# Kernel optimization log

Measured on AMD Instinct MI355X. Metric: run time of the kernel, lower is better.

## Reference

```python
import jax, jax.numpy as jnp
import numpy as np
import math

LMAX = 2
NUM_Z = 4
N_NODES = 20000
N_GRAPHS = 5000
N_EDGES = 320000
# irreps as (mul, l, parity)
IR_SH   = [(1, 0, 1), (1, 1, -1), (1, 2, 1)]
IR_ATTR = [(NUM_Z**2, 0, 1), (NUM_Z**2, 1, -1), (NUM_Z**2, 2, 1)]
IR_MID  = [(64, 0, 1), (24, 1, 1), (24, 1, -1), (16, 2, 1), (16, 2, -1)]
IR_OUT  = [(1, 0, -1), (6, 0, 1)]


def _cg(j1, j2, j3, m1, m2, m3):
    if m1 + m2 != m3:
        return 0.0
    f = math.factorial
    pre = math.sqrt((2 * j3 + 1) * f(j3 + j1 - j2) * f(j3 - j1 + j2) * f(j1 + j2 - j3) / f(j1 + j2 + j3 + 1))
    pre *= math.sqrt(f(j3 + m3) * f(j3 - m3) * f(j1 - m1) * f(j1 + m1) * f(j2 - m2) * f(j2 + m2))
    s = 0.0
    for k in range(max(0, j2 - j3 - m1, j1 - j3 + m2), min(j1 + j2 - j3, j1 - m1, j2 + m2) + 1):
        s += (-1) ** k / (f(k) * f(j1 + j2 - j3 - k) * f(j1 - m1 - k) * f(j2 + m2 - k) * f(j3 - j2 + m1 + k) * f(j3 - j1 - m2 + k))
    return pre * s


def _u(l):
    # complex -> real spherical harmonics change of basis, m = -l..l
    U = np.zeros((2 * l + 1, 2 * l + 1), dtype=complex)
    for m in range(-l, l + 1):
        if m > 0:
            U[m + l, -m + l] = 1 / math.sqrt(2)
            U[m + l, m + l] = (-1) ** m / math.sqrt(2)
        elif m == 0:
            U[l, l] = 1.0
        else:
            U[m + l, m + l] = 1j / math.sqrt(2)
            U[m + l, -m + l] = -1j * (-1) ** (-m) / math.sqrt(2)
    return U


def _w3j(l1, l2, l3):
    C = np.zeros((2 * l1 + 1, 2 * l2 + 1, 2 * l3 + 1))
    for m1 in range(-l1, l1 + 1):
        for m2 in range(-l2, l2 + 1):
            m3 = m1 + m2
            if -l3 <= m3 <= l3:
                C[m1 + l1, m2 + l2, m3 + l3] = _cg(l1, l2, l3, m1, m2, m3)
    T = np.einsum('am,bn,co,mno->abc', _u(l1), _u(l2), _u(l3).conj(), C.astype(complex))
    T = T.real if np.abs(T.real).max() >= np.abs(T.imag).max() else T.imag
    return (T / np.linalg.norm(T)).astype(np.float32)  # Frobenius norm 1, e3nn convention


W3J = {(a, b, c): _w3j(a, b, c) for a in range(3) for b in range(3) for c in range(3) if abs(a - b) <= c <= a + b}


def _slices(ir):
    s = [0]
    for m, l, _ in ir:
        s.append(s[-1] + m * (2 * l + 1))
    return s


def _paths(ir1, ir2, iro):
    paths = []
    fan = [0] * len(iro)
    off = 0
    for a, (m1, l1, p1) in enumerate(ir1):
        for b, (m2, l2, p2) in enumerate(ir2):
            for c, (m3, l3, p3) in enumerate(iro):
                if p1 * p2 == p3 and abs(l1 - l2) <= l3 <= l1 + l2:
                    paths.append((a, b, c, off))
                    fan[c] += m1 * m2
                    off += m1 * m2 * m3
    return paths, fan, off


def _fctp(x1, x2, w, ir1, ir2, iro):
    # FullyConnectedTensorProduct: 'uvw' weighted Clebsch-Gordan contraction per path
    s1, s2 = _slices(ir1), _slices(ir2)
    paths, fan, _ = _paths(ir1, ir2, iro)
    E = x1.shape[0]
    out = [jnp.zeros((E, m * (2 * l + 1)), x1.dtype) for m, l, _ in iro]
    for a, b, c, off in paths:
        m1, l1, _ = ir1[a]
        m2, l2, _ = ir2[b]
        m3, l3, _ = iro[c]
        W = w[off:off + m1 * m2 * m3].reshape(m1, m2, m3)
        C = jnp.asarray(W3J[(l1, l2, l3)], x1.dtype)
        xa = x1[:, s1[a]:s1[a + 1]].reshape(E, m1, 2 * l1 + 1)
        xb = x2[:, s2[b]:s2[b + 1]].reshape(E, m2, 2 * l2 + 1)
        alpha = math.sqrt(2 * l3 + 1) / math.sqrt(fan[c])
        y = jnp.einsum('eui,evj,ijk,uvw->ewk', xa, xb, C, W)
        out[c] = out[c] + (alpha * y).reshape(E, -1)
    return jnp.concatenate(out, axis=1)


def _sh(v):
    # component-normalized harmonic polynomials for l=0,1,2 (normalize=False)
    x, y, z = v[:, 0], v[:, 1], v[:, 2]
    r2 = x * x + y * y + z * z
    s3, s15, s5 = math.sqrt(3.0), math.sqrt(15.0), math.sqrt(5.0)
    sh1 = s3 * jnp.stack([y, z, x], axis=1)
    sh2 = jnp.stack([s15 * x * y, s15 * y * z, 0.5 * s5 * (3 * z * z - r2), s15 * x * z, 0.5 * s15 * (x * x - y * y)], axis=1)
    return jnp.concatenate([jnp.ones_like(x)[:, None], sh1, sh2], axis=1)  # [E, 9]


def _forward(pos, w_tp1, w_tp2, z, batch, edge_src, edge_dst):
    E = edge_src.shape[0]
    ev = pos[edge_src] - pos[edge_dst]
    sh = _sh(ev)
    zz = NUM_Z * z[edge_src] + z[edge_dst]
    zzf = jax.nn.one_hot(zz, NUM_Z ** 2, dtype=sh.dtype) * NUM_Z  # [E, 16]
    # 'uvu' TensorProduct of (16x0e) with sh: outer product per l block
    blocks = [(0, 1), (1, 4), (4, 9)]
    edge_attr = jnp.concatenate([(zzf[:, :, None] * sh[:, None, a:b]).reshape(E, -1) for a, b in blocks], axis=1)
    inv_nn = 1.0 / math.sqrt(3.0)  # num_neighbors = 3
    node = jax.ops.segment_sum(sh, edge_dst, num_segments=N_NODES) * inv_nn
    ef = _fctp(node[edge_src], edge_attr, w_tp1, IR_SH, IR_ATTR, IR_MID)
    node = jax.ops.segment_sum(ef, edge_dst, num_segments=N_NODES) * inv_nn
    ef = _fctp(node[edge_src], edge_attr, w_tp2, IR_MID, IR_ATTR, IR_OUT)
    node = jax.ops.segment_sum(ef, edge_dst, num_segments=N_NODES) * inv_nn
    return jax.ops.segment_sum(node, batch, num_segments=N_GRAPHS) * 0.5  # num_nodes = 4


def setup_inputs() -> dict:
    key = jax.random.key(0)
    k = jax.random.split(key, 7)
    _, _, n1 = _paths(IR_SH, IR_ATTR, IR_MID)
    _, _, n2 = _paths(IR_MID, IR_ATTR, IR_OUT)
    return {
        'pos': jax.random.normal(k[0], (N_NODES, 3), jnp.float32),
        'z': jax.random.randint(k[1], (N_NODES,), 0, NUM_Z, jnp.int32),
        'batch': jnp.sort(jax.random.randint(k[2], (N_NODES,), 0, N_GRAPHS, jnp.int32)),
        'edge_src': jax.random.randint(k[3], (N_EDGES,), 0, N_NODES, jnp.int32),
        'edge_dst': jax.random.randint(k[4], (N_EDGES,), 0, N_NODES, jnp.int32),
        'w_tp1': jax.random.normal(k[5], (n1,), jnp.float32),
        'w_tp2': jax.random.normal(k[6], (n2,), jnp.float32),
    }


def reference(pos, z, batch, edge_src, edge_dst, w_tp1, w_tp2):
    return _forward(pos, w_tp1, w_tp2, z, batch, edge_src, edge_dst)
```

## Files before the change

### kernel.cpp

```cpp
#include <hip/hip_runtime.h>


#define N_EDGES   320000
#define NN_NODES  20000
#define NN_GRAPHS 5000

__device__ __forceinline__ void sh_from_vec(float x, float y, float z,
                                            float* B1, float* B2) {
    const float s3   = 1.7320508075688772f;
    const float s15  = 3.8729833462074170f;
    const float s5h  = 1.1180339887498949f;
    const float s15h = 1.9364916731037085f;
    B1[0] = s3 * y; B1[1] = s3 * z; B1[2] = s3 * x;
    float r2 = x * x + y * y + z * z;
    B2[0] = s15 * x * y;
    B2[1] = s15 * y * z;
    B2[2] = s5h * (3.f * z * z - r2);
    B2[3] = s15 * x * z;
    B2[4] = s15h * (x * x - y * y);
}

__global__ __launch_bounds__(256) void k_zero(const float* __restrict__ pos,
                                              int* __restrict__ counts,
                                              float* __restrict__ out,
                                              float4* __restrict__ pos4) {
    int tid = blockIdx.x * blockDim.x + threadIdx.x;
    int stride = gridDim.x * blockDim.x;
    for (int i = tid; i < NN_NODES; i += stride) counts[i] = 0;
    for (int i = tid; i < NN_GRAPHS * 7; i += stride) out[i] = 0.f;
    for (int i = tid; i < NN_NODES; i += stride) {
        float4 p;
        p.x = pos[3 * i]; p.y = pos[3 * i + 1]; p.z = pos[3 * i + 2]; p.w = 0.f;
        pos4[i] = p;
    }
}

__global__ __launch_bounds__(256) void k_hist(const int* __restrict__ edst,
                                              int* __restrict__ counts) {
    int e = blockIdx.x * blockDim.x + threadIdx.x;
    if (e < N_EDGES) atomicAdd(&counts[edst[e]], 1);
}

__global__ __launch_bounds__(1024) void k_scan(const int* __restrict__ counts,
                                               int* __restrict__ start,
                                               int* __restrict__ cursor) {
    __shared__ int sdata[1024];
    __shared__ int carry;
    int tid = threadIdx.x;
    if (tid == 0) carry = 0;
    __syncthreads();
    for (int base = 0; base < NN_NODES; base += 1024) {
        int i = base + tid;
        int v = (i < NN_NODES) ? counts[i] : 0;
        sdata[tid] = v;
        __syncthreads();
        for (int off = 1; off < 1024; off <<= 1) {
            int t = (tid >= off) ? sdata[tid - off] : 0;
            __syncthreads();
            sdata[tid] += t;
            __syncthreads();
        }
        int incl = sdata[tid];
        int c = carry;
        if (i < NN_NODES) {
            int excl = c + incl - v;
            start[i] = excl;
            cursor[i] = excl;
        }
        __syncthreads();
        if (tid == 0) carry = c + sdata[1023];
        __syncthreads();
    }
    if (tid == 0) start[NN_NODES] = carry;
}

__global__ __launch_bounds__(256) void k_fill(const int* __restrict__ esrc,
                                              const int* __restrict__ edst,
                                              const int* __restrict__ zarr,
                                              int* __restrict__ cursor,
                                              int* __restrict__ csr) {
    int e = blockIdx.x * blockDim.x + threadIdx.x;
    if (e >= N_EDGES) return;
    int d = edst[e];
    int s = esrc[e];
    int q = 4 * zarr[s] + zarr[d];
    int p = atomicAdd(&cursor[d], 1);
    csr[p] = s | (q << 16) | ((d & 15) << 20);
}

__global__ __launch_bounds__(256) void k_wprep(const float* __restrict__ w2,
                                               float* __restrict__ w2p) {
    const float cT0f =  0.02830690f;
    const float cT1f = -0.02635231f;
    const float cT2f = -0.01634300f;
    const float cT3f =  0.01265893f;
    const float cT4f =  0.02041241f;
    int idx = blockIdx.x * 256 + threadIdx.x;
    if (idx >= 16 * 64 * 64) return;
    int jj = idx & 63;
    int u  = (idx >> 6) & 63;
    int q  = idx >> 12;
    float v = 0.f;
    if (jj < 6) {
        v = cT0f * w2[(u * 16 + q) * 6 + jj];
    } else if (jj < 9) {
        if (u < 24) v = cT1f * w2[6144 + u * 16 + q];
    } else if (jj < 27) {
        int w = (jj - 9) % 6;
        if (u < 24) v = cT2f * w2[6528 + (u * 16 + q) * 6 + w];
    } else if (jj < 57) {
        int w = (jj - 27) % 6;
        if (u < 16) v = cT3f * w2[8832 + (u * 16 + q) * 6 + w];
    } else if (jj < 62) {
        if (u < 16) v = cT4f * w2[10368 + u * 16 + q];
    }
    w2p[idx] = v;
}

__global__ __launch_bounds__(256) void k_nodesh(const float4* __restrict__ pos4,
                                                const int* __restrict__ start,
                                                const int* __restrict__ csr,
                                                float* __restrict__ node_sh) {
    __shared__ float ns[16][12];
    int t = threadIdx.x;
    if (t < 192) ns[t / 12][t % 12] = 0.f;
    __syncthreads();
    int nbase = blockIdx.x * 16;
    int e0 = start[nbase], e1 = start[nbase + 16];
    for (int idx = e0 + t; idx < e1; idx += 256) {
        int pk = csr[idx];
        int s = pk & 0xFFFF;
        int r = (pk >> 20) & 15;
        float4 pd = pos4[nbase + r];
        float4 ps = pos4[s];
        float x = ps.x - pd.x;
        float y = ps.y - pd.y;
        float z = ps.z - pd.z;
        float B1[3], B2[5];
        sh_from_vec(x, y, z, B1, B2);
        float* nr = &ns[r][0];
        atomicAdd(nr + 0, 1.f);
        atomicAdd(nr + 1, B1[0]); atomicAdd(nr + 2, B1[1]); atomicAdd(nr + 3, B1[2]);
        atomicAdd(nr + 4, B2[0]); atomicAdd(nr + 5, B2[1]); atomicAdd(nr + 6, B2[2]);
        atomicAdd(nr + 7, B2[3]); atomicAdd(nr + 8, B2[4]);
    }
    __syncthreads();
    if (t < 144) {
        int r = t / 9, c = t % 9;
        const float inv_nn = 0.57735026918962576f;
        node_sh[(size_t)(nbase + r) * 12 + c] = ns[r][c] * inv_nn;
    }
}

__global__ __launch_bounds__(512, 6) void k_mid(const float4* __restrict__ pos4,
                                                const float* __restrict__ node_sh,
                                                const int* __restrict__ start,
                                                const int* __restrict__ csr,
                                                const float* __restrict__ w1,
                                                const int* __restrict__ zarr,
                                                const float* __restrict__ w2p,
                                                float* __restrict__ tab) {
    __shared__ float Gl[8 * 816];
    __shared__ float smid[8][368];
    __shared__ int szl[8];
    int t = threadIdx.x;
    int nbase = blockIdx.x * 8;
    for (int i = t; i < 8 * 816; i += 512) Gl[i] = 0.f;
    if (t < 8) szl[t] = zarr[nbase + t];
    __syncthreads();

    int e0 = start[nbase], e1 = start[nbase + 8];

    const float r3  = 0.57735026918962576f;
    const float r5  = 0.44721359549995794f;
    const float r6  = 0.40824829046386302f;
    const float r10 = 0.31622776601683794f;
    const float s30 = 0.18257418583505536f;
    const float rt3 = 1.7320508075688772f;
    const float c222 = 0.58554004376911990f;
    const float q6 = 0.40824829046386302f;
    const float h6 = 0.20412414523193151f;
    const float h2 = 0.35355339059327376f;
    const float r2c = 0.70710678118654752f;

    for (int idx = e0 + t; idx < e1; idx += 512) {
        int pk = csr[idx];
        int s = pk & 0xFFFF;
        int q = (pk >> 16) & 15;
        int r = (pk >> 20) & 7;
        float4 pd = pos4[nbase + r];
        float4 ps = pos4[s];
        float x = ps.x - pd.x;
        float y = ps.y - pd.y;
        float z = ps.z - pd.z;
        float B1[3], B2[5];
        sh_from_vec(x, y, z, B1, B2);
        const float4 nv0 = *(const float4*)(node_sh + s * 12);
        const float4 nv1 = *(const float4*)(node_sh + s * 12 + 4);
        float a0 = nv0.x;
        float A1[3] = {nv0.y, nv0.z, nv0.w};
        float A2[5] = {nv1.x, nv1.y, nv1.z, nv1.w, node_sh[s * 12 + 8]};
        float* gr = Gl + r * 816 + q * 51;

        atomicAdd(gr + 0, a0);
        atomicAdd(gr + 1, a0 * B1[0] * r3);
        atomicAdd(gr + 2, a0 * B1[1] * r3);
        atomicAdd(gr + 3, a0 * B1[2] * r3);
        atomicAdd(gr + 4, a0 * B2[0] * r5);
        atomicAdd(gr + 5, a0 * B2[1] * r5);
        atomicAdd(gr + 6, a0 * B2[2] * r5);
        atomicAdd(gr + 7, a0 * B2[3] * r5);
        atomicAdd(gr + 8, a0 * B2[4] * r5);
        atomicAdd(gr + 9,  A1[0] * r3);
        atomicAdd(gr + 10, A1[1] * r3);
        atomicAdd(gr + 11, A1[2] * r3);
        atomicAdd(gr + 12, -r3 * (A1[0] * B1[0] + A1[1] * B1[1] + A1[2] * B1[2]));
        atomicAdd(gr + 13, -r6 * (A1[1] * B1[2] - A1[2] * B1[1]));
        atomicAdd(gr + 14, -r6 * (A1[2] * B1[0] - A1[0] * B1[2]));
        atomicAdd(gr + 15, -r6 * (A1[0] * B1[1] - A1[1] * B1[0]));
        atomicAdd(gr + 16, r10 * (A1[0] * B1[2] + A1[2] * B1[0]));
        atomicAdd(gr + 17, r10 * (A1[0] * B1[1] + A1[1] * B1[0]));
        atomicAdd(gr + 18, s30 * (2.f * A1[1] * B1[1] - A1[0] * B1[0] - A1[2] * B1[2]));
        atomicAdd(gr + 19, r10 * (A1[1] * B1[2] + A1[2] * B1[1]));
        atomicAdd(gr + 20, r10 * (A1[2] * B1[2] - A1[0] * B1[0]));
        {
            float Byy = -B2[2] * q6 - B2[4] * r2c;
            float Bzz = 2.f * B2[2] * q6;
            float Bxx = -B2[2] * q6 + B2[4] * r2c;
            float Bxy = B2[0] * r2c;
            float Byz = B2[1] * r2c;
            float Bxz = B2[3] * r2c;
            atomicAdd(gr + 21, -r5 * (Byy * A1[0] + Byz * A1[1] + Bxy * A1[2]));
            atomicAdd(gr + 22, -r5 * (Byz * A1[0] + Bzz * A1[1] + Bxz * A1[2]));
            atomicAdd(gr + 23, -r5 * (Bxy * A1[0] + Bxz * A1[1] + Bxx * A1[2]));
        }
        atomicAdd(gr + 24, -s30 * (B2[1] * A1[0] - B2[3] * A1[2] + 2.f * B2[4] * A1[1]));
        atomicAdd(gr + 25, -s30 * (-B2[0] * A1[0] - rt3 * B2[2] * A1[2] + B2[3] * A1[1] - B2[4] * A1[2]));
        atomicAdd(gr + 26, -s30 * (rt3 * B2[1] * A1[2] - rt3 * B2[3] * A1[0]));
        atomicAdd(gr + 27, -s30 * (B2[0] * A1[2] - B2[1] * A1[1] + rt3 * B2[2] * A1[0] - B2[4] * A1[0]));
        atomicAdd(gr + 28, -s30 * (-2.f * B2[0] * A1[1] + B2[1] * A1[2] + B2[3] * A1[0]));
        atomicAdd(gr + 29, A2[0] * r5);
        atomicAdd(gr + 30, A2[1] * r5);
        atomicAdd(gr + 31, A2[2] * r5);
        atomicAdd(gr + 32, A2[3] * r5);
        atomicAdd(gr + 33, A2[4] * r5);
        {
            float Ayy = -A2[2] * q6 - A2[4] * r2c;
            float Azz = 2.f * A2[2] * q6;
            float Axx = -A2[2] * q6 + A2[4] * r2c;
            float Axy = A2[0] * r2c;
            float Ayz = A2[1] * r2c;
            float Axz = A2[3] * r2c;
            atomicAdd(gr + 34, -r5 * (Ayy * B1[0] + Ayz * B1[1] + Axy * B1[2]));
            atomicAdd(gr + 35, -r5 * (Ayz * B1[0] + Azz * B1[1] + Axz * B1[2]));
            atomicAdd(gr + 36, -r5 * (Axy * B1[0] + Axz * B1[1] + Axx * B1[2]));
        }
        atomicAdd(gr + 37, s30 * (A2[1] * B1[0] - A2[3] * B1[2] + 2.f * A2[4] * B1[1]));
        atomicAdd(gr + 38, s30 * (-A2[0] * B1[0] - rt3 * A2[2] * B1[2] + A2[3] * B1[1] - A2[4] * B1[2]));
        atomicAdd(gr + 39, s30 * (rt3 * A2[1] * B1[2] - rt3 * A2[3] * B1[0]));
        atomicAdd(gr + 40, s30 * (A2[0] * B1[2] - A2[1] * B1[1] + rt3 * A2[2] * B1[0] - A2[4] * B1[0]));
        atomicAdd(gr + 41, s30 * (-2.f * A2[0] * B1[1] + A2[1] * B1[2] + A2[3] * B1[0]));
        atomicAdd(gr + 42, r5 * (A2[0] * B2[0] + A2[1] * B2[1] + A2[2] * B2[2] +
                                 A2[3] * B2[3] + A2[4] * B2[4]));
        atomicAdd(gr + 43, s30 * (-A2[0] * B2[1] + A2[1] * B2[0] +
                                  rt3 * (A2[2] * B2[3] - A2[3] * B2[2]) +
                                  A2[3] * B2[4] - A2[4] * B2[3]));
        atomicAdd(gr + 44, s30 * (-2.f * A2[0] * B2[4] + 2.f * A2[4] * B2[0] -
                                  A2[1] * B2[3] + A2[3] * B2[1]));
        atomicAdd(gr + 45, s30 * (A2[0] * B2[3] - A2[3] * B2[0] +
                                  rt3 * (A2[1] * B2[2] - A2[2] * B2[1]) +
                                  A2[1] * B2[4] - A2[4] * B2[1]));
        atomicAdd(gr + 46, -c222 * (-q6 * (A2[0] * B2[2] + A2[2] * B2[0]) +
                                    h2 * (A2[1] * B2[3] + A2[3] * B2[1])));
        atomicAdd(gr + 47, -c222 * (h6 * (A2[1] * B2[2] + A2[2] * B2[1]) -
                                    h2 * (A2[1] * B2[4] + A2[4] * B2[1]) +
                                    h2 * (A2[0] * B2[3] + A2[3] * B2[0])));
        atomicAdd(gr + 48, -c222 * (q6 * (A2[2] * B2[2] - A2[0] * B2[0] - A2[4] * B2[4]) +
                                    h6 * (A2[1] * B2[1] + A2[3] * B2[3])));
        atomicAdd(gr + 49, -c222 * (h6 * (A2[3] * B2[2] + A2[2] * B2[3]) +
                                    h2 * (A2[3] * B2[4] + A2[4] * B2[3]) +
                                    h2 * (A2[0] * B2[1] + A2[1] * B2[0])));
        atomicAdd(gr + 50, -c222 * (-q6 * (A2[4] * B2[2] + A2[2] * B2[4]) +
                                    h2 * (A2[3] * B2[3] - A2[1] * B2[1])));
    }
    __syncthreads();

    int j = t;
    if (j < 368) {
        float acc[8] = {0.f, 0.f, 0.f, 0.f, 0.f, 0.f, 0.f, 0.f};
        if (j < 64) {
            int w = j;
            for (int q = 0; q < 16; q++) {
                float wa = w1[q * 64 + w];
                float wb = w1[2048 + q * 64 + w];
                float wc = w1[5248 + q * 64 + w];
                const float* Gq = Gl + q * 51;
#pragma unroll
                for (int r2 = 0; r2 < 8; r2++) {
                    const float* gq = Gq + r2 * 816;
                    acc[r2] += gq[0] * wa + gq[12] * wb + gq[42] * wc;
                }
            }
#pragma unroll
            for (int r2 = 0; r2 < 8; r2++) smid[r2][j] = 0.33333333333333333f * acc[r2];
        } else if (j < 136) {
            int tt = j - 64, w = tt / 3, k = tt - 3 * w;
            for (int q = 0; q < 16; q++) {
                float wa = w1[3072 + q * 24 + w];
                float wb = w1[6272 + q * 24 + w];
                const float* Gq = Gl + q * 51;
#pragma unroll
                for (int r2 = 0; r2 < 8; r2++) {
                    const float* gq = Gq + r2 * 816;
                    acc[r2] += gq[13 + k] * wa + gq[43 + k] * wb;
                }
            }
#pragma unroll
            for (int r2 = 0; r2 < 8; r2++) smid[r2][j] = 0.70710678118654752f * acc[r2];
        } else if (j < 208) {
            int tt = j - 136, w = tt / 3, k = tt - 3 * w;
            for (int q = 0; q < 16; q++) {
                float wa = w1[1024 + q * 24 + w];
                float wb = w1[1664 + q * 24 + w];
                float wc = w1[3712 + q * 24 + w];
                float wd = w1[4608 + q * 24 + w];
                const float* Gq = Gl + q * 51;
#pragma unroll
                for (int r2 = 0; r2 < 8; r2++) {
                    const float* gq = Gq + r2 * 816;
                    acc[r2] += gq[1 + k] * wa + gq[9 + k] * wb +
                               gq[21 + k] * wc + gq[34 + k] * wd;
                }
            }
#pragma unroll
            for (int r2 = 0; r2 < 8; r2++) smid[r2][j] = 0.5f * acc[r2];
        } else if (j < 288) {
            int tt = j - 208, w = tt / 5, k = tt - 5 * w;
            for (int q = 0; q < 16; q++) {
                float wa = w1[1408 + q * 16 + w];
                float wb = w1[3456 + q * 16 + w];
                float wc = w1[4352 + q * 16 + w];
                float wd = w1[6656 + q * 16 + w];
                const float* Gq = Gl + q * 51;
#pragma unroll
                for (int r2 = 0; r2 < 8; r2++) {
                    const float* gq = Gq + r2 * 816;
                    acc[r2] += gq[4 + k] * wa + gq[16 + k] * wb +
                               gq[29 + k] * wc + gq[46 + k] * wd;
                }
            }
#pragma unroll
            for (int r2 = 0; r2 < 8; r2++) smid[r2][j] = 0.64549722436790280f * acc[r2];
        } else {
            int tt = j - 288, w = tt / 5, k = tt - 5 * w;
            for (int q = 0; q < 16; q++) {
                float wa = w1[4096 + q * 16 + w];
                float wb = w1[4992 + q * 16 + w];
                const float* Gq = Gl + q * 51;
#pragma unroll
                for (int r2 = 0; r2 < 8; r2++) {
                    const float* gq = Gq + r2 * 816;
                    acc[r2] += gq[24 + k] * wa + gq[37 + k] * wb;
                }
            }
#pragma unroll
            for (int r2 = 0; r2 < 8; r2++) smid[r2][j] = 0.91287092917527690f * acc[r2];
        }
    }
    __syncthreads();

    {
        int wave = t >> 6;
        int lane = t & 63;
        int r = wave;
        int mbase, mstride, ulim;
        if (lane < 6)       { mbase = 0;                mstride = 1; ulim = 64; }
        else if (lane < 9)  { mbase = 64 + (lane - 6);  mstride = 3; ulim = 24; }
        else if (lane < 27) { mbase = 136 + (lane - 9) / 6;  mstride = 3; ulim = 24; }
        else if (lane < 57) { mbase = 208 + (lane - 27) / 6; mstride = 5; ulim = 16; }
        else if (lane < 62) { mbase = 288 + (lane - 57);     mstride = 5; ulim = 16; }
        else                { mbase = 0;                mstride = 0; ulim = 1; }
        int ulim1 = ulim - 1;
        const float* mr = &smid[r][0];
        int zs = szl[r];
        for (int zd = 0; zd < 4; zd++) {
            int q = 4 * zs + zd;
            const float* wp = w2p + (size_t)q * 4096 + lane;
            float s0 = 0.f, s1 = 0.f;
#pragma unroll 8
            for (int u = 0; u < 64; u += 2) {
                int um0 = (u < ulim) ? u : ulim1;
                int um1 = (u + 1 < ulim) ? u + 1 : ulim1;
                s0 += mr[mbase + mstride * um0] * wp[u * 64];
                s1 += mr[mbase + mstride * um1] * wp[(u + 1) * 64];
            }
            tab[((size_t)(nbase + r) * 4 + zd) * 64 + lane] = s0 + s1;
        }
    }
}

__global__ __launch_bounds__(512, 8) void k_out(const float4* __restrict__ pos4,
                                                const int* __restrict__ zarr,
                                                const int* __restrict__ batch,
                                                const int* __restrict__ start,
                                                const int* __restrict__ csr,
                                                const float* __restrict__ tab,
                                                float* __restrict__ out) {
    int wave = threadIdx.x >> 6;
    int lane = threadIdx.x & 63;
    int n = blockIdx.x * 8 + wave;
    float4 pd = pos4[n];
    int zd = zarr[n];
    int s0 = start[n], s1 = start[n + 1];

    int fsel, oidx;
    if (lane < 6)       { fsel = 0;                  oidx = lane + 1; }
    else if (lane < 9)  { fsel = 1 + (lane - 6);     oidx = 0; }
    else if (lane < 27) { fsel = 1 + (lane - 9) / 6; oidx = (lane - 9) % 6 + 1; }
    else if (lane < 57) { fsel = 4 + (lane - 27) / 6; oidx = (lane - 27) % 6 + 1; }
    else if (lane < 62) { fsel = 4 + (lane - 57);    oidx = 0; }
    else                { fsel = -1;                 oidx = 7; }
    float f0 = (fsel == 0) ? 1.f : 0.f;
    float f1 = (fsel == 1) ? 1.f : 0.f;
    float f2 = (fsel == 2) ? 1.f : 0.f;
    float f3 = (fsel == 3) ? 1.f : 0.f;
    float f4 = (fsel == 4) ? 1.f : 0.f;
    float f5 = (fsel == 5) ? 1.f : 0.f;
    float f6 = (fsel == 6) ? 1.f : 0.f;
    float f7 = (fsel == 7) ? 1.f : 0.f;
    float f8 = (fsel == 8) ? 1.f : 0.f;

    float acc = 0.f;
    for (int idx = s0; idx < s1; ++idx) {
        int pk = csr[idx];
        pk = __builtin_amdgcn_readfirstlane(pk);
        int s = pk & 0xFFFF;
        float T = tab[((size_t)s * 4 + zd) * 64 + lane];
        float4 ps = pos4[s];
        float x = ps.x - pd.x;
        float y = ps.y - pd.y;
        float z = ps.z - pd.z;
        float B1[3], B2[5];
        sh_from_vec(x, y, z, B1, B2);
        float factor = f0 + f1 * B1[0] + f2 * B1[1] + f3 * B1[2]
                     + f4 * B2[0] + f5 * B2[1] + f6 * B2[2]
                     + f7 * B2[3] + f8 * B2[4];
        acc += T * factor;
    }

    float ov[7];
#pragma unroll
    for (int w = 0; w < 7; w++) ov[w] = (oidx == w) ? acc : 0.f;
#pragma unroll
    for (int off = 32; off > 0; off >>= 1)
#pragma unroll
        for (int w = 0; w < 7; w++) ov[w] += __shfl_down(ov[w], off, 64);
    if (lane == 0) {
        float* og = out + batch[n] * 7;
#pragma unroll
        for (int w = 0; w < 7; w++) atomicAdd(og + w, ov[w]);
    }
}

extern "C" void kernel_launch(void* const* d_in, const int* in_sizes, int n_in,
                              void* d_out, int out_size, void* d_ws, size_t ws_size,
                              hipStream_t stream) {
    const float* pos  = (const float*)d_in[0];
    const int*   z    = (const int*)d_in[1];
    const int*   bat  = (const int*)d_in[2];
    const int*   esrc = (const int*)d_in[3];
    const int*   edst = (const int*)d_in[4];
    const float* w1   = (const float*)d_in[5];
    const float* w2   = (const float*)d_in[6];
    float* out = (float*)d_out;

    int*   wsI = (int*)d_ws;
    float* wsF = (float*)d_ws;
    int* counts  = wsI + 0;
    int* start   = wsI + 32768;
    int* cursor  = wsI + 65536;
    int* csr     = wsI + 98304;
    float4* pos4   = (float4*)(wsF + 425984);
    float* node_sh = wsF + 524288;
    float* w2p     = wsF + 786432;
    float* tab     = wsF + 1048576;

    k_zero<<<64, 256, 0, stream>>>(pos, counts, out, pos4);
    k_hist<<<(N_EDGES + 255) / 256, 256, 0, stream>>>(edst, counts);
    k_scan<<<1, 1024, 0, stream>>>(counts, start, cursor);
    k_fill<<<(N_EDGES + 255) / 256, 256, 0, stream>>>(esrc, edst, z, cursor, csr);
    k_wprep<<<256, 256, 0, stream>>>(w2, w2p);
    k_nodesh<<<NN_NODES / 16, 256, 0, stream>>>(pos4, start, csr, node_sh);
    k_mid<<<NN_NODES / 8, 512, 0, stream>>>(pos4, node_sh, start, csr, w1, z, w2p, tab);
    k_out<<<NN_NODES / 8, 512, 0, stream>>>(pos4, z, bat, start, csr, tab, out);
}
```

Baseline: 392.1 us.

## Exploit fixed destination species to shrink shared accumulator and skip zero bins

Each destination node has one species, so only 4 of the 16 (src, dst) species bins in the per-node edge accumulator can ever be nonzero. The shared accumulator is shrunk to 4 source-species bins per node, which cuts shared-memory zeroing and footprint and may allow more resident blocks. The weight contraction skips the 12 empty bins through a block-uniform check on each node's species, read with readfirstlane. Correctness relies on the packed edge index holding the source species in bits 18-19.

Result: faster. 377.8 us (-3.7%).

```diff
diff --git a/kernel.cpp b/kernel.cpp
--- a/kernel.cpp
+++ b/kernel.cpp
@@ -160,12 +160,12 @@
                                                 const int* __restrict__ zarr,
                                                 const float* __restrict__ w2p,
                                                 float* __restrict__ tab) {
-    __shared__ float Gl[8 * 816];
+    __shared__ float Gl[8 * 204];
     __shared__ float smid[8][368];
     __shared__ int szl[8];
     int t = threadIdx.x;
     int nbase = blockIdx.x * 8;
-    for (int i = t; i < 8 * 816; i += 512) Gl[i] = 0.f;
+    for (int i = t; i < 8 * 204; i += 512) Gl[i] = 0.f;
     if (t < 8) szl[t] = zarr[nbase + t];
     __syncthreads();
 
@@ -186,7 +186,7 @@
     for (int idx = e0 + t; idx < e1; idx += 512) {
         int pk = csr[idx];
         int s = pk & 0xFFFF;
-        int q = (pk >> 16) & 15;
+        int zs = (pk >> 18) & 3;
         int r = (pk >> 20) & 7;
         float4 pd = pos4[nbase + r];
         float4 ps = pos4[s];
@@ -200,7 +200,7 @@
         float a0 = nv0.x;
         float A1[3] = {nv0.y, nv0.z, nv0.w};
         float A2[5] = {nv1.x, nv1.y, nv1.z, nv1.w, node_sh[s * 12 + 8]};
-        float* gr = Gl + r * 816 + q * 51;
+        float* gr = Gl + r * 204 + zs * 51;
 
         atomicAdd(gr + 0, a0);
         atomicAdd(gr + 1, a0 * B1[0] * r3);
@@ -285,6 +285,11 @@
     }
     __syncthreads();
 
+    int zrs[8];
+#pragma unroll
+    for (int r2 = 0; r2 < 8; r2++)
+        zrs[r2] = __builtin_amdgcn_readfirstlane(szl[r2]);
+
     int j = t;
     if (j < 368) {
         float acc[8] = {0.f, 0.f, 0.f, 0.f, 0.f, 0.f, 0.f, 0.f};
@@ -294,11 +299,14 @@
                 float wa = w1[q * 64 + w];
                 float wb = w1[2048 + q * 64 + w];
                 float wc = w1[5248 + q * 64 + w];
-                const float* Gq = Gl + q * 51;
+                int zdq = q & 3;
+                const float* Gq = Gl + (q >> 2) * 51;
 #pragma unroll
                 for (int r2 = 0; r2 < 8; r2++) {
-                    const float* gq = Gq + r2 * 816;
-                    acc[r2] += gq[0] * wa + gq[12] * wb + gq[42] * wc;
+                    if (zrs[r2] == zdq) {
+                        const float* gq = Gq + r2 * 204;
+                        acc[r2] += gq[0] * wa + gq[12] * wb + gq[42] * wc;
+                    }
                 }
             }
 #pragma unroll
@@ -308,11 +316,14 @@
             for (int q = 0; q < 16; q++) {
                 float wa = w1[3072 + q * 24 + w];
                 float wb = w1[6272 + q * 24 + w];
-                const float* Gq = Gl + q * 51;
+                int zdq = q & 3;
+                const float* Gq = Gl + (q >> 2) * 51;
 #pragma unroll
                 for (int r2 = 0; r2 < 8; r2++) {
-                    const float* gq = Gq + r2 * 816;
-                    acc[r2] += gq[13 + k] * wa + gq[43 + k] * wb;
+                    if (zrs[r2] == zdq) {
+                        const float* gq = Gq + r2 * 204;
+                        acc[r2] += gq[13 + k] * wa + gq[43 + k] * wb;
+                    }
                 }
             }
 #pragma unroll
@@ -324,12 +335,15 @@
                 float wb = w1[1664 + q * 24 + w];
                 float wc = w1[3712 + q * 24 + w];
                 float wd = w1[4608 + q * 24 + w];
-                const float* Gq = Gl + q * 51;
+                int zdq = q & 3;
+                const float* Gq = Gl + (q >> 2) * 51;
 #pragma unroll
                 for (int r2 = 0; r2 < 8; r2++) {
-                    const float* gq = Gq + r2 * 816;
-                    acc[r2] += gq[1 + k] * wa + gq[9 + k] * wb +
-                               gq[21 + k] * wc + gq[34 + k] * wd;
+                    if (zrs[r2] == zdq) {
+                        const float* gq = Gq + r2 * 204;
+                        acc[r2] += gq[1 + k] * wa + gq[9 + k] * wb +
+                                   gq[21 + k] * wc + gq[34 + k] * wd;
+                    }
                 }
             }
 #pragma unroll
@@ -341,12 +355,15 @@
                 float wb = w1[3456 + q * 16 + w];
                 float wc = w1[4352 + q * 16 + w];
                 float wd = w1[6656 + q * 16 + w];
-                const float* Gq = Gl + q * 51;
+                int zdq = q & 3;
+                const float* Gq = Gl + (q >> 2) * 51;
 #pragma unroll
                 for (int r2 = 0; r2 < 8; r2++) {
-                    const float* gq = Gq + r2 * 816;
-                    acc[r2] += gq[4 + k] * wa + gq[16 + k] * wb +
-                               gq[29 + k] * wc + gq[46 + k] * wd;
+                    if (zrs[r2] == zdq) {
+                        const float* gq = Gq + r2 * 204;
+                        acc[r2] += gq[4 + k] * wa + gq[16 + k] * wb +
+                                   gq[29 + k] * wc + gq[46 + k] * wd;
+                    }
                 }
             }
 #pragma unroll
@@ -356,11 +373,14 @@
             for (int q = 0; q < 16; q++) {
                 float wa = w1[4096 + q * 16 + w];
                 float wb = w1[4992 + q * 16 + w];
-                const float* Gq = Gl + q * 51;
+                int zdq = q & 3;
+                const float* Gq = Gl + (q >> 2) * 51;
 #pragma unroll
                 for (int r2 = 0; r2 < 8; r2++) {
-                    const float* gq = Gq + r2 * 816;
-                    acc[r2] += gq[24 + k] * wa + gq[37 + k] * wb;
+                    if (zrs[r2] == zdq) {
+                        const float* gq = Gq + r2 * 204;
+                        acc[r2] += gq[24 + k] * wa + gq[37 + k] * wb;
+                    }
                 }
             }
 #pragma unroll
@@ -382,7 +402,7 @@
         else                { mbase = 0;                mstride = 0; ulim = 1; }
         int ulim1 = ulim - 1;
         const float* mr = &smid[r][0];
-        int zs = szl[r];
+        int zs = zrs[r];
         for (int zd = 0; zd < 4; zd++) {
             int q = 4 * zs + zd;
             const float* wp = w2p + (size_t)q * 4096 + lane;
```
